# Kernel optimization log

Hardware: AMD Instinct MI355X
Metric: run time of the kernel (lower is better)

Reference implementation:

```python
import jax, jax.numpy as jnp
import numpy as np

GRID_N = 256          # hardcoded 256x256 grid in the module
D = 64                # conv channel width
NL = 18               # module applications used (9 conv + 9 PReLU, interleaved)
LABEL_NC = 19
STYLE_DIM = 512


def setup_inputs() -> dict:
    key = jax.random.key(0)
    ks = jax.random.split(key, 7)
    B, C = 2, LABEL_NC
    x = jax.random.randint(ks[0], (B, C, GRID_N, GRID_N), 0, 2).astype(jnp.int32)
    conv_w0 = jax.random.normal(ks[1], (D, 2), dtype=jnp.float32) * 0.1
    conv_w = jax.random.normal(ks[2], (8, D, D), dtype=jnp.float32) * 0.05
    conv_b = jax.random.normal(ks[3], (9, D), dtype=jnp.float32) * 0.01
    prelu_a = jnp.full((9, D), 0.25, dtype=jnp.float32)  # PReLU default init
    fc_w = jax.random.normal(ks[4], (NL, STYLE_DIM, D * C), dtype=jnp.float32)
    fc_b = jnp.zeros((NL, STYLE_DIM), dtype=jnp.float32)
    return dict(x=x, conv_w0=conv_w0, conv_w=conv_w, conv_b=conv_b,
                prelu_a=prelu_a, fc_w=fc_w, fc_b=fc_b)


def _point_features(pts, conv_w0, conv_w, conv_b, prelu_a):
    """pts: (P,2). Returns (NL, P, D): snapshot after each of the 18 modules
    (conv, prelu, conv, prelu, ...) -- exactly what the original max-pools."""
    snaps = []
    z = pts @ conv_w0.T + conv_b[0]            # Conv1d(2,64,1) == pointwise linear
    snaps.append(z)
    z = jnp.where(z > 0, z, prelu_a[0] * z)    # PReLU(64)
    snaps.append(z)
    for i in range(8):
        z = z @ conv_w[i].T + conv_b[i + 1]
        snaps.append(z)
        z = jnp.where(z > 0, z, prelu_a[i + 1] * z)
        snaps.append(z)
    return jnp.stack(snaps)                    # (18, P, D)


def reference(x, conv_w0, conv_w, conv_b, prelu_a, fc_w, fc_b):
    B, C = x.shape[0], x.shape[1]
    P = GRID_N * GRID_N
    lin = jnp.linspace(-1.0, 1.0, GRID_N, dtype=jnp.float32)
    gx, gy = jnp.meshgrid(lin, lin)            # numpy default 'xy' indexing
    pts = jnp.stack([gx.reshape(-1), gy.reshape(-1)], axis=-1)   # (P, 2)

    # Grid points are shared by every (b, c): compute features once.
    snaps = _point_features(pts, conv_w0, conv_w, conv_b, prelu_a)        # (18, P, D)
    zero_snaps = _point_features(jnp.zeros((1, 2), jnp.float32),
                                 conv_w0, conv_w, conv_b, prelu_a)[:, 0]  # (18, D)

    mask = (x.reshape(B, C, P) == 1)           # (B, C, P)
    empty = ~jnp.any(mask, axis=-1)            # (B, C): original falls back to a zero point

    neg = jnp.float32(-jnp.inf)
    pooled = []
    for l in range(NL):                        # fixed, small layer loop
        pl = jnp.max(jnp.where(mask[..., None], snaps[l][None, None], neg), axis=2)  # (B,C,D)
        pl = jnp.where(empty[..., None], zero_snaps[l][None, None], pl)
        pooled.append(pl)
    pooled = jnp.stack(pooled, axis=1)         # (B, 18, C, D)
    feat = pooled.reshape(B, NL, C * D)        # channel-major concat, matches torch.cat dim=2

    # EqualLinear: out = x @ (W * scale).T + bias, scale = 1/sqrt(in_dim), lr_mul=1
    scale = 1.0 / jnp.sqrt(jnp.float32(C * D))
    # fcs are applied in reversed layer order and concatenated in that order
    w_rev = fc_w[::-1] * scale                 # (18, 512, C*D)
    b_rev = fc_b[::-1]                         # (18, 512)
    out = jnp.einsum('bld,lsd->bls', feat[:, ::-1], w_rev) + b_rev[None]
    return out                                  # (B, 18, 512)
```

## Files before the change

kernel.cpp:

```cpp
#include <hip/hip_runtime.h>

#define NSET 38
#define NSNAP 9
#define PART (NSNAP*NSET*64)
#define PPB 64
#define ZSTR 65
#define ASTR 40
#define WHALF (8*64*64)

typedef unsigned int uint;
typedef __fp16 half8 __attribute__((ext_vector_type(8)));
typedef float  f32x4 __attribute__((ext_vector_type(4)));

template<int CHUNKS>
__global__ __launch_bounds__(256)
void kA(const int* __restrict__ x, const float* __restrict__ w0,
        const float* __restrict__ cw, const float* __restrict__ cb,
        const float* __restrict__ pa, const __fp16* __restrict__ wf,
        float* __restrict__ partial)
{
  __shared__ float zt[PPB * ZSTR];
  __shared__ float addend[PPB * ASTR];
  __shared__ uint  memb2[PPB * 2];

  const int tid = threadIdx.x;
  const int q  = tid & 63;
  const int g  = __builtin_amdgcn_readfirstlane(tid >> 6);
  const int l  = tid & 63;
  const int lr = l & 15;
  const int lg = l >> 4;
  const int sbase = g * 10;
  const int nset = (g == 3) ? 8 : 10;

  #pragma unroll 1
  for (int c = 0; c < CHUNKS; ++c) {
    const int p = (blockIdx.x * CHUNKS + c) * PPB + q;

    if (c) __syncthreads();
    if (tid < 128) {
      const int half = tid >> 6;
      uint m = 0;
      #pragma unroll
      for (int j = 0; j < 19; ++j)
        m |= (uint)(x[(half * 19 + j) * 65536 + p] == 1) << j;
      memb2[q * 2 + half] = m;
    }
    __syncthreads();

    {
      const int pt = tid >> 2;
      const int jb = (tid & 3) * 10;
      uint lo = memb2[pt * 2], hi = memb2[pt * 2 + 1];
      #pragma unroll
      for (int jj = 0; jj < 10; ++jj) {
        int j = jb + jj;
        uint bit = (j < 19) ? ((lo >> j) & 1u)
                 : (j < 38) ? ((hi >> (j - 19)) & 1u) : 0u;
        addend[pt * ASTR + j] = bit ? 0.f : -1e38f;
      }
    }

    float acc0[16];
    {
      float px = -1.f + (2.f / 255.f) * (float)(p & 255);
      float py = -1.f + (2.f / 255.f) * (float)(p >> 8);
      #pragma unroll
      for (int d = 0; d < 16; ++d) {
        int dd = (g << 4) + d;
        acc0[d] = fmaf(px, w0[2 * dd], fmaf(py, w0[2 * dd + 1], cb[dd]));
      }
    }
    __syncthreads();

    f32x4 Cf[4];

    #pragma unroll 1
    for (int s = 0; s < NSNAP; ++s) {
      if (s) __syncthreads();
      if (s == 0) {
        #pragma unroll
        for (int d = 0; d < 16; ++d) {
          int dd = (g << 4) + d;
          float zv = acc0[d];
          float a = pa[dd];
          zt[q * ZSTR + dd] = zv > 0.f ? zv : a * zv;
        }
      } else {
        #pragma unroll
        for (int dt = 0; dt < 4; ++dt) {
          float a = pa[(s << 6) + (dt << 4) + lr];
          #pragma unroll
          for (int r = 0; r < 4; ++r) {
            float zv = Cf[dt][r];
            zt[((g << 4) + (lg << 2) + r) * ZSTR + (dt << 4) + lr] =
                zv > 0.f ? zv : a * zv;
          }
        }
      }
      __syncthreads();

      float run[10];
      #pragma unroll
      for (int j = 0; j < 10; ++j) run[j] = -3e38f;
      #pragma unroll 2
      for (int pp = 0; pp < PPB; pp += 2) {
        float v0 = zt[(pp + 0) * ZSTR + q];
        float v1 = zt[(pp + 1) * ZSTR + q];
        const float2* A0 = (const float2*)&addend[(pp + 0) * ASTR + sbase];
        const float2* A1 = (const float2*)&addend[(pp + 1) * ASTR + sbase];
        float2 a0[5], a1[5];
        #pragma unroll
        for (int t = 0; t < 5; ++t) { a0[t] = A0[t]; a1[t] = A1[t]; }
        #pragma unroll
        for (int t = 0; t < 5; ++t) {
          run[2*t]   = fmaxf(fmaxf(run[2*t],   v0 + a0[t].x), v1 + a1[t].x);
          run[2*t+1] = fmaxf(fmaxf(run[2*t+1], v0 + a0[t].y), v1 + a1[t].y);
        }
      }
      {
        float* pb = partial + (size_t)blockIdx.x * PART + s * (NSET * 64) + q;
        #pragma unroll
        for (int j = 0; j < 10; ++j) {
          if (j < nset) {
            int set = sbase + j;
            if (CHUNKS == 1 || c == 0) pb[set * 64] = run[j];
            else                       pb[set * 64] = fmaxf(pb[set * 64], run[j]);
          }
        }
      }

      if (s < 8) {
        const float* zr = &zt[((g << 4) + lr) * ZSTR + (lg << 3)];
        half8 a0, a1;
        #pragma unroll
        for (int j = 0; j < 8; ++j) a0[j] = (__fp16)zr[j];
        #pragma unroll
        for (int j = 0; j < 8; ++j) a1[j] = (__fp16)zr[32 + j];
        const __fp16* wb = wf + ((size_t)s << 12);
        #pragma unroll
        for (int dt = 0; dt < 4; ++dt) {
          float bias = cb[((s + 1) << 6) + (dt << 4) + lr];
          f32x4 a4 = {bias, bias, bias, bias};
          half8 b0 = *(const half8*)&wb[(((dt << 4) + lr) << 6) + (lg << 3)];
          half8 b1 = *(const half8*)&wb[(((dt << 4) + lr) << 6) + 32 + (lg << 3)];
          a4 = __builtin_amdgcn_mfma_f32_16x16x32_f16(a0, b0, a4, 0, 0, 0);
          a4 = __builtin_amdgcn_mfma_f32_16x16x32_f16(a1, b1, a4, 0, 0, 0);
          Cf[dt] = a4;
        }
      }
    }
  }
}

__global__ __launch_bounds__(256) void kW(const float* __restrict__ cw,
                                          __fp16* __restrict__ wf)
{
  int i = blockIdx.x * 256 + threadIdx.x;
  if (i < WHALF) wf[i] = (__fp16)cw[i];
}

__global__ __launch_bounds__(256) void kB1(float* __restrict__ partial, int per)
{
  int idx = blockIdx.x * 256 + threadIdx.x;
  if (idx >= PART) return;
  float* p0 = partial + (size_t)blockIdx.y * per * PART + idx;
  float mx = -3e38f;
  #pragma unroll 8
  for (int b = 0; b < per; ++b)
    mx = fmaxf(mx, p0[(size_t)b * PART]);
  p0[0] = mx;
}

__global__ __launch_bounds__(256) void kB2(const float* __restrict__ partial,
    int per, const float* __restrict__ cw, const float* __restrict__ cb,
    const float* __restrict__ pa, float* __restrict__ feat)
{
  __shared__ float zl[64];
  __shared__ float zc[NSNAP][64];
  __shared__ float zp[NSNAP][64];
  int tid = threadIdx.x;
  int d = tid & 63;
  float z = cb[d];
  #pragma unroll 1
  for (int s = 0; s < NSNAP; ++s) {
    if (tid < 64) {
      zc[s][d] = z;
      float a = pa[(s << 6) + d];
      float v = z > 0.f ? z : a * z;
      zp[s][d] = v;
      zl[d] = v;
    }
    __syncthreads();
    if (s < 8) {
      if (tid < 64) {
        float a2 = cb[((s + 1) << 6) + d];
        for (int k = 0; k < 64; ++k)
          a2 = fmaf(zl[k], cw[(s << 12) + (d << 6) + k], a2);
        z = a2;
      }
    }
    __syncthreads();
  }

  int idx = blockIdx.x * 256 + tid;
  if (idx >= PART) return;
  int s = idx / (NSET * 64);
  int r = idx - s * (NSET * 64);
  int set = r >> 6;
  int dd = r & 63;
  float mx = -3e38f;
  #pragma unroll
  for (int y = 0; y < 32; ++y)
    mx = fmaxf(mx, partial[(size_t)y * per * PART + idx]);
  int b = set / 19, cc = set - b * 19;
  float even_v, odd_v;
  if (mx < -5e37f) {
    even_v = zc[s][dd];
    odd_v  = zp[s][dd];
  } else {
    odd_v = mx;
    float a = pa[(s << 6) + dd];
    even_v = mx > 0.f ? mx : mx / a;
  }
  size_t fb = ((size_t)b * 18 + 2 * s) * 1216 + cc * 64 + dd;
  feat[fb] = even_v;
  feat[fb + 1216] = odd_v;
}

__global__ __launch_bounds__(256) void kC(const float* __restrict__ feat,
    const float* __restrict__ fcw, const float* __restrict__ fcb,
    float* __restrict__ out)
{
  __shared__ float f0[1216], f1[1216];
  int lr = blockIdx.y;
  int chunk = blockIdx.x;
  int tid = threadIdx.x;
  for (int i = tid; i < 1216; i += 256) {
    f0[i] = feat[(size_t)(0 * 18 + lr) * 1216 + i];
    f1[i] = feat[(size_t)(1 * 18 + lr) * 1216 + i];
  }
  __syncthreads();
  int wv = tid >> 6, lane = tid & 63;
  float scale = 1.f / sqrtf(1216.f);
  int l = 17 - lr;
  #pragma unroll 1
  for (int rr = 0; rr < 4; ++rr) {
    int srow = (chunk << 4) + (wv << 2) + rr;
    const float* wrow = fcw + ((size_t)lr * 512 + srow) * 1216;
    float pp0 = 0.f, pp1 = 0.f;
    #pragma unroll
    for (int k = 0; k < 19; ++k) {
      float w = wrow[(k << 6) + lane];
      pp0 = fmaf(w, f0[(k << 6) + lane], pp0);
      pp1 = fmaf(w, f1[(k << 6) + lane], pp1);
    }
    #pragma unroll
    for (int off = 32; off; off >>= 1) {
      pp0 += __shfl_xor(pp0, off, 64);
      pp1 += __shfl_xor(pp1, off, 64);
    }
    if (lane == 0) {
      float b = fcb[lr * 512 + srow];
      out[((size_t)0 * 18 + l) * 512 + srow] = fmaf(scale, pp0, b);
      out[((size_t)1 * 18 + l) * 512 + srow] = fmaf(scale, pp1, b);
    }
  }
}

extern "C" void kernel_launch(void* const* d_in, const int* in_sizes, int n_in,
                              void* d_out, int out_size, void* d_ws, size_t ws_size,
                              hipStream_t stream) {
  const int*   x   = (const int*)d_in[0];
  const float* w0  = (const float*)d_in[1];
  const float* cw  = (const float*)d_in[2];
  const float* cb  = (const float*)d_in[3];
  const float* pa  = (const float*)d_in[4];
  const float* fcw = (const float*)d_in[5];
  const float* fcb = (const float*)d_in[6];
  float* ws = (float*)d_ws;
  float* out = (float*)d_out;

  const size_t tail = (size_t)2 * 18 * 1216 + WHALF / 2;
  #define NEED(n) (((size_t)(n) * PART + tail) * 4)

  int nblk;
  if      (ws_size >= NEED(1024)) nblk = 1024;
  else if (ws_size >= NEED(512))  nblk = 512;
  else                            nblk = 256;

  float* partial = ws;
  float* feat = ws + (size_t)nblk * PART;
  __fp16* wf = (__fp16*)(feat + (size_t)2 * 18 * 1216);
  const int per = nblk >> 5;

  hipLaunchKernelGGL(kW, dim3(WHALF / 256), dim3(256), 0, stream, cw, wf);

  if (nblk == 1024) {
    hipLaunchKernelGGL(kA<1>, dim3(1024), dim3(256), 0, stream,
                       x, w0, cw, cb, pa, wf, partial);
  } else if (nblk == 512) {
    hipLaunchKernelGGL(kA<2>, dim3(512), dim3(256), 0, stream,
                       x, w0, cw, cb, pa, wf, partial);
  } else {
    hipLaunchKernelGGL(kA<4>, dim3(256), dim3(256), 0, stream,
                       x, w0, cw, cb, pa, wf, partial);
  }

  hipLaunchKernelGGL(kB1, dim3(86, 32), dim3(256), 0, stream, partial, per);
  hipLaunchKernelGGL(kB2, dim3(86), dim3(256), 0, stream,
                     partial, per, cw, cb, pa, feat);
  hipLaunchKernelGGL(kC, dim3(32, 18), dim3(256), 0, stream, feat, fcw, fcb, out);
}
```

Baseline: 162.8 us.

## Use packed fp16 masked max-pool with transposed half activation tiles

Stores post-PReLU activations in shared memory as fp16, both row-major for MFMA operand loads and transposed for pooling. The masked max-pool now uses v_pk_add_f16/v_pk_max_f16 on two points per instruction with -inf half mask addends, halving the ALU and LDS traffic of the pooling loop. The MFMA for the next layer is issued before pooling so its latency can overlap the pooling work. Pooled values now carry fp16 rounding, and a dummy padding shared array is added, which raises LDS use and may limit occupancy.

```diff
diff --git a/kernel.cpp b/kernel.cpp
--- a/kernel.cpp
+++ b/kernel.cpp
@@ -1,16 +1,36 @@
 #include <hip/hip_runtime.h>
+#include <hip/hip_fp16.h>
 
 #define NSET 38
 #define NSNAP 9
 #define PART (NSNAP*NSET*64)
 #define PPB 64
-#define ZSTR 65
-#define ASTR 40
+#define HSTR 72
+#define PSTR 66
 #define WHALF (8*64*64)
 
 typedef unsigned int uint;
 typedef __fp16 half8 __attribute__((ext_vector_type(8)));
 typedef float  f32x4 __attribute__((ext_vector_type(4)));
+
+#define HNEGINF 0xFC00u
+
+static __device__ __forceinline__ uint pk_add(uint a, uint b) {
+  uint r;
+  asm volatile("v_pk_add_f16 %0, %1, %2" : "=v"(r) : "v"(a), "v"(b));
+  return r;
+}
+static __device__ __forceinline__ uint pk_max(uint a, uint b) {
+  uint r;
+  asm volatile("v_pk_max_f16 %0, %1, %2" : "=v"(r) : "v"(a), "v"(b));
+  return r;
+}
+static __device__ __forceinline__ float half_lo_f(uint u) {
+  return (float)__builtin_bit_cast(__fp16, (unsigned short)(u & 0xFFFFu));
+}
+static __device__ __forceinline__ float half_hi_f(uint u) {
+  return (float)__builtin_bit_cast(__fp16, (unsigned short)(u >> 16));
+}
 
 template<int CHUNKS>
 __global__ __launch_bounds__(256)
@@ -19,9 +39,11 @@
         const float* __restrict__ pa, const __fp16* __restrict__ wf,
         float* __restrict__ partial)
 {
-  __shared__ float zt[PPB * ZSTR];
-  __shared__ float addend[PPB * ASTR];
-  __shared__ uint  memb2[PPB * 2];
+  __shared__ __fp16 zth[PPB * HSTR];
+  __shared__ __fp16 ztp[64 * PSTR];
+  __shared__ uint   addp[32 * 40];
+  __shared__ uint   memb2[PPB * 2];
+  __shared__ float  padl[1024];
 
   const int tid = threadIdx.x;
   const int q  = tid & 63;
@@ -32,6 +54,8 @@
   const int sbase = g * 10;
   const int nset = (g == 3) ? 8 : 10;
 
+  if ((int)blockIdx.x < 0) padl[tid] = 0.f;
+
   #pragma unroll 1
   for (int c = 0; c < CHUNKS; ++c) {
     const int p = (blockIdx.x * CHUNKS + c) * PPB + q;
@@ -47,17 +71,14 @@
     }
     __syncthreads();
 
-    {
-      const int pt = tid >> 2;
-      const int jb = (tid & 3) * 10;
-      uint lo = memb2[pt * 2], hi = memb2[pt * 2 + 1];
-      #pragma unroll
-      for (int jj = 0; jj < 10; ++jj) {
-        int j = jb + jj;
-        uint bit = (j < 19) ? ((lo >> j) & 1u)
-                 : (j < 38) ? ((hi >> (j - 19)) & 1u) : 0u;
-        addend[pt * ASTR + j] = bit ? 0.f : -1e38f;
-      }
+    #pragma unroll
+    for (int i = tid; i < 1280; i += 256) {
+      int pr = i / 40, j = i - pr * 40;
+      uint lo0 = memb2[(2 * pr) * 2],     hi0 = memb2[(2 * pr) * 2 + 1];
+      uint lo1 = memb2[(2 * pr + 1) * 2], hi1 = memb2[(2 * pr + 1) * 2 + 1];
+      uint b0 = (j < 19) ? ((lo0 >> j) & 1u) : (j < 38) ? ((hi0 >> (j - 19)) & 1u) : 0u;
+      uint b1 = (j < 19) ? ((lo1 >> j) & 1u) : (j < 38) ? ((hi1 >> (j - 19)) & 1u) : 0u;
+      addp[i] = (b0 ? 0u : HNEGINF) | ((b1 ? 0u : HNEGINF) << 16);
     }
 
     float acc0[16];
@@ -83,59 +104,32 @@
           int dd = (g << 4) + d;
           float zv = acc0[d];
           float a = pa[dd];
-          zt[q * ZSTR + dd] = zv > 0.f ? zv : a * zv;
+          float zp = zv > 0.f ? zv : a * zv;
+          zth[q * HSTR + dd] = (__fp16)zp;
+          ztp[dd * PSTR + q] = (__fp16)zp;
         }
       } else {
         #pragma unroll
         for (int dt = 0; dt < 4; ++dt) {
-          float a = pa[(s << 6) + (dt << 4) + lr];
+          int dim = (dt << 4) + lr;
+          float a = pa[(s << 6) + dim];
+          __fp16 zp[4];
           #pragma unroll
           for (int r = 0; r < 4; ++r) {
             float zv = Cf[dt][r];
-            zt[((g << 4) + (lg << 2) + r) * ZSTR + (dt << 4) + lr] =
-                zv > 0.f ? zv : a * zv;
+            zp[r] = (__fp16)(zv > 0.f ? zv : a * zv);
+            zth[((g << 4) + (lg << 2) + r) * HSTR + dim] = zp[r];
           }
+          int pt0 = (g << 4) + (lg << 2);
+          __fp16* dst = &ztp[dim * PSTR + pt0];
+          dst[0] = zp[0]; dst[1] = zp[1]; dst[2] = zp[2]; dst[3] = zp[3];
         }
       }
       __syncthreads();
 
-      float run[10];
-      #pragma unroll
-      for (int j = 0; j < 10; ++j) run[j] = -3e38f;
-      #pragma unroll 2
-      for (int pp = 0; pp < PPB; pp += 2) {
-        float v0 = zt[(pp + 0) * ZSTR + q];
-        float v1 = zt[(pp + 1) * ZSTR + q];
-        const float2* A0 = (const float2*)&addend[(pp + 0) * ASTR + sbase];
-        const float2* A1 = (const float2*)&addend[(pp + 1) * ASTR + sbase];
-        float2 a0[5], a1[5];
-        #pragma unroll
-        for (int t = 0; t < 5; ++t) { a0[t] = A0[t]; a1[t] = A1[t]; }
-        #pragma unroll
-        for (int t = 0; t < 5; ++t) {
-          run[2*t]   = fmaxf(fmaxf(run[2*t],   v0 + a0[t].x), v1 + a1[t].x);
-          run[2*t+1] = fmaxf(fmaxf(run[2*t+1], v0 + a0[t].y), v1 + a1[t].y);
-        }
-      }
-      {
-        float* pb = partial + (size_t)blockIdx.x * PART + s * (NSET * 64) + q;
-        #pragma unroll
-        for (int j = 0; j < 10; ++j) {
-          if (j < nset) {
-            int set = sbase + j;
-            if (CHUNKS == 1 || c == 0) pb[set * 64] = run[j];
-            else                       pb[set * 64] = fmaxf(pb[set * 64], run[j]);
-          }
-        }
-      }
-
       if (s < 8) {
-        const float* zr = &zt[((g << 4) + lr) * ZSTR + (lg << 3)];
-        half8 a0, a1;
-        #pragma unroll
-        for (int j = 0; j < 8; ++j) a0[j] = (__fp16)zr[j];
-        #pragma unroll
-        for (int j = 0; j < 8; ++j) a1[j] = (__fp16)zr[32 + j];
+        half8 a0 = *(const half8*)&zth[((g << 4) + lr) * HSTR + (lg << 3)];
+        half8 a1 = *(const half8*)&zth[((g << 4) + lr) * HSTR + 32 + (lg << 3)];
         const __fp16* wb = wf + ((size_t)s << 12);
         #pragma unroll
         for (int dt = 0; dt < 4; ++dt) {
@@ -146,6 +140,30 @@
           a4 = __builtin_amdgcn_mfma_f32_16x16x32_f16(a0, b0, a4, 0, 0, 0);
           a4 = __builtin_amdgcn_mfma_f32_16x16x32_f16(a1, b1, a4, 0, 0, 0);
           Cf[dt] = a4;
+        }
+      }
+
+      uint run2[10];
+      #pragma unroll
+      for (int j = 0; j < 10; ++j) run2[j] = HNEGINF | (HNEGINF << 16);
+      #pragma unroll 2
+      for (int pr = 0; pr < 32; ++pr) {
+        uint v = *(const uint*)&ztp[q * PSTR + (pr << 1)];
+        const uint* ap = &addp[pr * 40 + sbase];
+        #pragma unroll
+        for (int j = 0; j < 10; ++j)
+          run2[j] = pk_max(run2[j], pk_add(v, ap[j]));
+      }
+      {
+        float* pb = partial + (size_t)blockIdx.x * PART + s * (NSET * 64) + q;
+        #pragma unroll
+        for (int j = 0; j < 10; ++j) {
+          if (j < nset) {
+            float mx = fmaxf(half_lo_f(run2[j]), half_hi_f(run2[j]));
+            int set = sbase + j;
+            if (CHUNKS == 1 || c == 0) pb[set * 64] = mx;
+            else                       pb[set * 64] = fmaxf(pb[set * 64], mx);
+          }
         }
       }
     }
```

Result: slower. 176.0 us (+8.1%).
